# Performance work log

Measured on AMD Instinct MI355X. Metric: run time of the kernel, lower is better.

## Reference

```python
import jax, jax.numpy as jnp
from jax import lax
import numpy as np

B, S, T = 128, 256, 256
VOCAB, EMBED, ENC, DEC, DOF, LOOKBACK = 32000, 256, 256, 512, 4, 4


def setup_inputs() -> dict:
    key = jax.random.key(0)
    ks = jax.random.split(key, 20)
    w = lambda k, shape: jax.random.normal(k, shape, jnp.float32) * 0.05
    return {
        "in_seq": jax.random.randint(ks[0], (B, S), 0, VOCAB),
        "tgt_seq": jax.random.normal(ks[1], (B, T, DOF), jnp.float32),
        "lengths": jnp.full((B,), S, dtype=jnp.int32),
        "embedding": w(ks[2], (VOCAB, EMBED)),
        "enc_Wih_f": w(ks[3], (4 * ENC, EMBED)),
        "enc_Whh_f": w(ks[4], (4 * ENC, ENC)),
        "enc_b_f": w(ks[5], (4 * ENC,)),
        "enc_Wih_b": w(ks[6], (4 * ENC, EMBED)),
        "enc_Whh_b": w(ks[7], (4 * ENC, ENC)),
        "enc_b_b": w(ks[8], (4 * ENC,)),
        "dec_Wih": w(ks[9], (4 * DEC, DEC + LOOKBACK * DOF)),
        "dec_Whh": w(ks[10], (4 * DEC, DEC)),
        "dec_b": w(ks[11], (4 * DEC,)),
        "W_src": w(ks[12], (DEC, 2 * ENC)),
        "W_ctx": w(ks[13], (DEC, 2 * ENC + DEC)),
        "W_out": w(ks[14], (DOF, DEC)),
        "b_out": w(ks[15], (DOF,)),
    }


def _lstm_cell(x, h, c, Wih, Whh, b):
    # PyTorch gate order: i, f, g, o
    g = x @ Wih.T + h @ Whh.T + b
    i, f, gg, o = jnp.split(g, 4, axis=-1)
    c_new = jax.nn.sigmoid(f) * c + jax.nn.sigmoid(i) * jnp.tanh(gg)
    h_new = jax.nn.sigmoid(o) * jnp.tanh(c_new)
    return h_new, c_new


def _scan_lstm(xs, Wih, Whh, b, reverse=False):
    # xs: [T, B, E] -> hidden states [T, B, H] (aligned to original time order)
    Bsz, H = xs.shape[1], Whh.shape[1]
    h0 = jnp.zeros((Bsz, H), xs.dtype)

    def step(carry, x):
        h, c = carry
        h, c = _lstm_cell(x, h, c, Wih, Whh, b)
        return (h, c), h

    _, hs = lax.scan(step, (h0, h0), xs, reverse=reverse)
    return hs


def reference(in_seq, tgt_seq, lengths, embedding,
              enc_Wih_f, enc_Whh_f, enc_b_f,
              enc_Wih_b, enc_Whh_b, enc_b_b,
              dec_Wih, dec_Whh, dec_b,
              W_src, W_ctx, W_out, b_out):
    Bsz, Tlen = tgt_seq.shape[0], tgt_seq.shape[1]
    # ----- encoder (bi-LSTM, eval mode: dropout off, zero initial state) -----
    emb = embedding[in_seq]              # [B,S,E]
    xs = jnp.swapaxes(emb, 0, 1)         # [S,B,E]
    hf = _scan_lstm(xs, enc_Wih_f, enc_Whh_f, enc_b_f, reverse=False)
    hb = _scan_lstm(xs, enc_Wih_b, enc_Whh_b, enc_b_b, reverse=True)
    enc_out = jnp.swapaxes(jnp.concatenate([hf, hb], axis=-1), 0, 1)  # [B,S,2H]
    enc_mask = (in_seq == 0)             # [B,S]
    # precompute attention source projection once (same math as per-step)
    proj = jnp.einsum('bse,de->bsd', enc_out, W_src)  # [B,S,DEC]
    # ----- teacher-forced lookback windows of target frames -----
    pad = jnp.concatenate([jnp.zeros((Bsz, LOOKBACK, DOF), tgt_seq.dtype), tgt_seq], axis=1)
    win = jnp.stack([pad[:, k:k + Tlen] for k in range(LOOKBACK)], axis=2)  # [B,T,LB,DOF]
    win = win.reshape(Bsz, Tlen, LOOKBACK * DOF)
    win_t = jnp.swapaxes(win, 0, 1)      # [T,B,LB*DOF]
    h0 = jnp.zeros((Bsz, DEC), tgt_seq.dtype)

    def step(carry, w_t):
        h, c, feed = carry
        x = jnp.concatenate([w_t, feed], axis=-1)         # [B, LB*DOF + DEC]
        h, c = _lstm_cell(x, h, c, dec_Wih, dec_Whh, dec_b)
        scores = jnp.einsum('bd,bsd->bs', h, proj)        # Luong general score
        scores = jnp.where(enc_mask, -jnp.inf, scores)
        aw = jax.nn.softmax(scores, axis=-1)              # [B,S]
        ctx = jnp.einsum('bs,bse->be', aw, enc_out)       # [B,2H]
        feed = jnp.tanh(jnp.concatenate([h, ctx], axis=-1) @ W_ctx.T)
        out = feed @ W_out.T + b_out                      # [B,DOF]
        return (h, c, feed), (out, aw)

    _, (outs, aws) = lax.scan(step, (h0, h0, h0), win_t)
    dec_outputs = jnp.swapaxes(outs, 0, 1)   # [B,T,DOF]
    attn_weights = jnp.swapaxes(aws, 0, 1)   # [B,T,S]
    outputs = jnp.concatenate(
        [jnp.tanh(dec_outputs[..., :-1]), jax.nn.relu(dec_outputs[..., -1:])], axis=-1)
    return outputs, attn_weights
```

## Files before the change

kernel.cpp:

```cpp
#include <hip/hip_runtime.h>
#include <stdint.h>

#define B 128
#define S 256
#define T 256
#define EMBED 256
#define ENC 256
#define DEC 512
#define DOF 4

typedef __attribute__((ext_vector_type(8))) short bf16x8;
typedef __attribute__((ext_vector_type(4))) float f32x4;

static __device__ __forceinline__ float bf2f(unsigned short u){
  union{uint32_t u;float f;}c; c.u = ((uint32_t)u)<<16; return c.f;
}
static __device__ __forceinline__ unsigned short f2bf(float f){
  union{float f;uint32_t u;}c; c.f=f; uint32_t u=c.u;
  u += 0x7fffu + ((u>>16)&1u);
  return (unsigned short)(u>>16);
}
static __device__ __forceinline__ void unp2(uint32_t w, float&a, float&b){
  union{uint32_t u;float f;}c1,c2; c1.u = w<<16; c2.u = w & 0xffff0000u; a=c1.f; b=c2.f;
}
static __device__ __forceinline__ float sigm(float x){ return 1.0f/(1.0f+__expf(-x)); }

static __device__ __forceinline__ unsigned long long ldc8(const void* p){
  return __hip_atomic_load((unsigned long long*)p, __ATOMIC_RELAXED, __HIP_MEMORY_SCOPE_AGENT);
}
static __device__ __forceinline__ void stc8(void* p, unsigned long long v){
  __hip_atomic_store((unsigned long long*)p, v, __ATOMIC_RELAXED, __HIP_MEMORY_SCOPE_AGENT);
}
static __device__ __forceinline__ void stc4(void* p, unsigned v){
  __hip_atomic_store((unsigned*)p, v, __ATOMIC_RELAXED, __HIP_MEMORY_SCOPE_AGENT);
}
static __device__ __forceinline__ void stc4f(float* p, float v){
  __hip_atomic_store((unsigned*)p, __float_as_uint(v), __ATOMIC_RELAXED, __HIP_MEMORY_SCOPE_AGENT);
}
static __device__ __forceinline__ float ldc4f(const float* p){
  return __uint_as_float(__hip_atomic_load((const unsigned*)p, __ATOMIC_RELAXED, __HIP_MEMORY_SCOPE_AGENT));
}
union F16x8 { unsigned long long q[2]; bf16x8 v; unsigned short s[8]; };
union Ubf   { bf16x8 v; uint32_t u[4]; unsigned short s[8]; };
static __device__ __forceinline__ bf16x8 ldfrag_c(const unsigned short* p){
  F16x8 u; u.q[0] = ldc8(p); u.q[1] = ldc8(p + 4); return u.v;
}
static __device__ __forceinline__ unsigned long long pack4bf(float a,float b,float c,float d){
  return (unsigned long long)f2bf(a) | ((unsigned long long)f2bf(b)<<16)
       | ((unsigned long long)f2bf(c)<<32) | ((unsigned long long)f2bf(d)<<48);
}

#define CLINE 32
#define A_OFF 0
#define C_OFF 64
#define F_OFF 128
#define PAIR_OFF 192
#define ENC_OFF 320
static __device__ __forceinline__ unsigned* cl(unsigned* c, int line){ return c + (size_t)line*CLINE; }

static __device__ __forceinline__ void bar_arr(unsigned* line){
  __builtin_amdgcn_s_waitcnt(0);
  __syncthreads();
  if (threadIdx.x == 0)
    __hip_atomic_fetch_add(line, 1u, __ATOMIC_RELAXED, __HIP_MEMORY_SCOPE_AGENT);
}
static __device__ __forceinline__ void barw(unsigned* set, unsigned target, int mask){
  if (threadIdx.x < 64){
    unsigned* p = set + (size_t)(threadIdx.x & mask)*CLINE;
    while (!__all((int)(__hip_atomic_load(p, __ATOMIC_RELAXED, __HIP_MEMORY_SCOPE_AGENT) >= target)))
      __builtin_amdgcn_s_sleep(1);
  }
  __syncthreads();
  asm volatile("" ::: "memory");
}
static __device__ __forceinline__ void pair_sync(unsigned* line, unsigned target){
  __builtin_amdgcn_s_waitcnt(0);
  __syncthreads();
  if (threadIdx.x == 0){
    __hip_atomic_fetch_add(line, 1u, __ATOMIC_RELAXED, __HIP_MEMORY_SCOPE_AGENT);
    while (__hip_atomic_load(line, __ATOMIC_RELAXED, __HIP_MEMORY_SCOPE_AGENT) < target)
      __builtin_amdgcn_s_sleep(1);
  }
  __syncthreads();
  asm volatile("" ::: "memory");
}

static __device__ __forceinline__ int enc_idx(int s, int c){
  return s*256 + (((c & 24) | ((c ^ s) & 7)) << 3);
}

__global__ __launch_bounds__(256,1) void k_encoder(
  const unsigned short* __restrict__ emb,
  const unsigned short* __restrict__ WF, const unsigned short* __restrict__ WB,
  const float* __restrict__ bF, const float* __restrict__ bB,
  unsigned short* __restrict__ hEnc,
  unsigned short* __restrict__ encOut,
  unsigned* __restrict__ cntBase)
{
  __shared__ __align__(16) unsigned short Ws[16*520];
  __shared__ __align__(16) float Gs[64*17];
  __shared__ float bsh[16];
  const int bid = blockIdx.x;
  const int dir = bid >> 7;
  const int mg  = (bid >> 6) & 1;
  const int ng  = bid & 63;
  const int tid = threadIdx.x;
  const int lane = tid & 63, w = tid >> 6;
  const int l16 = lane & 15, qd = lane >> 4;
  const int m_base = mg * 64;
  unsigned* mycnt = cntBase + (size_t)dir*16*CLINE;
  unsigned* myline = cl(mycnt, bid & 15);

  const unsigned short* Wg = (dir ? WB : WF) + (size_t)ng*16*512;
  for (int i = tid; i < 16*64; i += 256){
    const int r = i >> 6, s = i & 63;
    *(uint4*)&Ws[r*520 + s*8] = *(const uint4*)&Wg[r*512 + s*8];
  }
  if (tid < 16) bsh[tid] = (dir ? bB : bF)[ng*16 + tid];
  float c[4] = {0.f,0.f,0.f,0.f};
  __syncthreads();

  for (int t = 0; t < S; ++t){
    const int tt = dir ? (S-1-t) : t;
    const unsigned short* Ae = emb + ((size_t)tt*B + m_base + w*16 + l16)*256 + qd*8;
    bf16x8 av[8];
#pragma unroll
    for (int ks = 0; ks < 8; ++ks) av[ks] = *(const bf16x8*)(Ae + ks*32);
    if (t) barw(mycnt, (unsigned)(8u*(unsigned)t), 15);
    const unsigned short* Ah = hEnc + (((size_t)dir*2 + (size_t)(t&1))*B + m_base + w*16 + l16)*256 + qd*8;
    bf16x8 hf[8];
#pragma unroll
    for (int ks = 0; ks < 8; ++ks) hf[ks] = ldfrag_c(Ah + ks*32);
    f32x4 acc = (f32x4){0.f,0.f,0.f,0.f};
#pragma unroll
    for (int ks = 0; ks < 8; ++ks){
      bf16x8 bb = *(const bf16x8*)&Ws[l16*520 + ks*32 + qd*8];
      acc = __builtin_amdgcn_mfma_f32_16x16x32_bf16(av[ks], bb, acc, 0, 0, 0);
    }
#pragma unroll
    for (int ks = 0; ks < 8; ++ks){
      bf16x8 bb = *(const bf16x8*)&Ws[l16*520 + 256 + ks*32 + qd*8];
      acc = __builtin_amdgcn_mfma_f32_16x16x32_bf16(hf[ks], bb, acc, 0, 0, 0);
    }
    __syncthreads();
#pragma unroll
    for (int r = 0; r < 4; ++r)
      Gs[(w*16 + qd*4 + r)*17 + l16] = acc[r];
    __syncthreads();
    if (tid < 64){
      const int bl = tid;
      float hv[4];
#pragma unroll
      for (int u = 0; u < 4; ++u){
        const float gi = Gs[bl*17 + u*4 + 0] + bsh[u*4 + 0];
        const float gf = Gs[bl*17 + u*4 + 1] + bsh[u*4 + 1];
        const float gg = Gs[bl*17 + u*4 + 2] + bsh[u*4 + 2];
        const float go = Gs[bl*17 + u*4 + 3] + bsh[u*4 + 3];
        const float cn = sigm(gf)*c[u] + sigm(gi)*tanhf(gg);
        c[u] = cn;
        hv[u] = sigm(go)*tanhf(cn);
      }
      const int b2 = m_base + bl;
      const unsigned long long hq = pack4bf(hv[0],hv[1],hv[2],hv[3]);
      stc8(&hEnc[(((size_t)dir*2 + (size_t)((t+1)&1))*B + b2)*256 + ng*4], hq);
      *(unsigned long long*)&encOut[((size_t)b2*S + tt)*512 + dir*256 + ng*4] = hq;
    }
    bar_arr(myline);
  }
}

__global__ __launch_bounds__(256,2) void k_proj(
  const unsigned short* __restrict__ encOut,
  const unsigned short* __restrict__ WSP,
  unsigned short* __restrict__ proj)
{
  const int nb = blockIdx.x & 7;
  const int mt = blockIdx.x >> 3;
  const int tid = threadIdx.x;
  const int lane = tid & 63, w = tid >> 6;
  const int l16 = lane & 15, qd = lane >> 4;
  const int m0 = mt*64 + w*16;
  const unsigned short* Ap = encOut + ((size_t)m0 + l16)*512 + qd*8;
  bf16x8 av[16];
#pragma unroll
  for (int ks = 0; ks < 16; ++ks) av[ks] = *(const bf16x8*)(Ap + ks*32);
  for (int nn = 0; nn < 4; ++nn){
    const int qn = nb*4 + nn;
    const unsigned short* Bq = WSP + (size_t)qn*16*512 + (size_t)lane*8;
    f32x4 acc = (f32x4){0.f,0.f,0.f,0.f};
#pragma unroll
    for (int ks = 0; ks < 16; ++ks){
      bf16x8 bb = *(const bf16x8*)(Bq + (size_t)ks*512);
      acc = __builtin_amdgcn_mfma_f32_16x16x32_bf16(av[ks], bb, acc, 0, 0, 0);
    }
    const int d = qn*16 + l16, dh = d >> 8, dl = d & 255;
#pragma unroll
    for (int r = 0; r < 4; ++r){
      const int m = m0 + qd*4 + r;
      const int bb2 = m >> 8, s = m & 255;
      proj[(((size_t)bb2*2 + dh)*256 + s)*256 + dl] = f2bf(acc[r]);
    }
  }
}

__global__ __launch_bounds__(256,1) void k_decoder(
  const unsigned short* __restrict__ win,
  const unsigned short* __restrict__ WDx,
  const float* __restrict__ bD,
  const unsigned short* __restrict__ WCx,
  const unsigned short* __restrict__ projq,
  const unsigned short* __restrict__ encOut,
  const int* __restrict__ in_seq,
  const float* __restrict__ Wout, const float* __restrict__ bout,
  unsigned short* __restrict__ hdec,
  unsigned short* __restrict__ feed,
  unsigned short* __restrict__ ctxb,
  float* __restrict__ scp,
  float* __restrict__ out_main, float* __restrict__ out_attn,
  unsigned* __restrict__ cnts)
{
  __shared__ __align__(16) unsigned short encS[65536];
  __shared__ __align__(16) float scrf[1600];
  __shared__ float bsh[16];
  const int bid = blockIdx.x;
  const int b  = bid >> 1, eh = bid & 1;
  const int mg = bid & 1, ng = (bid >> 1) & 127;
  const int tid = threadIdx.x;
  const int lane = tid & 63, w = tid >> 6;
  const int l16 = lane & 15, qd = lane >> 4;
  const int m_base = mg*64;

  if (tid < 16) bsh[tid] = bD[ng*16 + tid];
  const int mymask = (in_seq[b*S + tid] == 0);
  {
    const unsigned short* Pq = projq + (((size_t)b*2 + eh)*256)*256;
    for (int i = 0; i < 32; ++i){
      const int s = i*8 + (tid>>5), cc = tid & 31;
      const uint4 v = *(const uint4*)&Pq[(size_t)s*256 + cc*8];
      *(uint4*)&encS[enc_idx(s, cc)] = v;
    }
  }
  bf16x8 ev[32];
  {
    const int cc = lane & 31, par = lane >> 5;
    const unsigned short* Ep = encOut + ((size_t)b*S)*512 + eh*256 + cc*8;
#pragma unroll
    for (int i2 = 0; i2 < 32; ++i2)
      ev[i2] = *(const bf16x8*)(Ep + (size_t)(w*64 + i2*2 + par)*512);
  }
  float c[4] = {0.f,0.f,0.f,0.f};
  __syncthreads();

  for (int t = 0; t < T; ++t){
    const int row = m_base + w*16 + l16;
    const unsigned short* Aw = win  + ((size_t)t*B + row)*64 + qd*8;
    const unsigned short* Af = feed + (size_t)row*512 + qd*8;
    const unsigned short* Ah = hdec + ((size_t)(t&1)*B + row)*512 + qd*8;
    const unsigned short* Bp = WDx + (size_t)ng*34*512 + (size_t)lane*8;
    f32x4 acc = (f32x4){0.f,0.f,0.f,0.f};
#pragma unroll
    for (int ch = 0; ch < 2; ++ch){
      bf16x8 hv[8];
#pragma unroll
      for (int i = 0; i < 8; ++i) hv[i] = ldfrag_c(Ah + (ch*8 + i)*32);
#pragma unroll
      for (int ks = 0; ks < 8; ++ks){
        bf16x8 bb = *(const bf16x8*)(Bp + (size_t)(18 + ch*8 + ks)*512);
        acc = __builtin_amdgcn_mfma_f32_16x16x32_bf16(hv[ks], bb, acc, 0, 0, 0);
      }
    }
    bf16x8 a0 = *(const bf16x8*)(Aw);
    bf16x8 a1 = *(const bf16x8*)(Aw + 32);
    if (t){
      if (bid & 1) barw(cl(cnts, F_OFF), (unsigned)t, 63);
      else         barw(cl(cnts, F_OFF), (unsigned)t, 31);
    }
    {
      bf16x8 b0 = *(const bf16x8*)(Bp);
      bf16x8 b1 = *(const bf16x8*)(Bp + 512);
      acc = __builtin_amdgcn_mfma_f32_16x16x32_bf16(a0, b0, acc, 0, 0, 0);
      acc = __builtin_amdgcn_mfma_f32_16x16x32_bf16(a1, b1, acc, 0, 0, 0);
    }
#pragma unroll
    for (int ch = 0; ch < 2; ++ch){
      bf16x8 av[8], bv[8];
#pragma unroll
      for (int i = 0; i < 8; ++i){
        av[i] = ldfrag_c(Af + (ch*8 + i)*32);
        bv[i] = *(const bf16x8*)(Bp + (size_t)(2 + ch*8 + i)*512);
      }
#pragma unroll
      for (int ks = 0; ks < 8; ++ks)
        acc = __builtin_amdgcn_mfma_f32_16x16x32_bf16(av[ks], bv[ks], acc, 0, 0, 0);
    }
    __syncthreads();
#pragma unroll
    for (int r = 0; r < 4; ++r)
      scrf[(w*16 + qd*4 + r)*17 + l16] = acc[r];
    __syncthreads();
    if (tid < 64){
      float hv[4];
#pragma unroll
      for (int u = 0; u < 4; ++u){
        const float gi = scrf[tid*17 + u*4 + 0] + bsh[u*4 + 0];
        const float gf = scrf[tid*17 + u*4 + 1] + bsh[u*4 + 1];
        const float gg = scrf[tid*17 + u*4 + 2] + bsh[u*4 + 2];
        const float go = scrf[tid*17 + u*4 + 3] + bsh[u*4 + 3];
        const float cn = sigm(gf)*c[u] + sigm(gi)*tanhf(gg);
        c[u] = cn;
        hv[u] = sigm(go)*tanhf(cn);
      }
      stc8(&hdec[((size_t)((t+1)&1)*B + m_base + tid)*512 + ng*4],
           pack4bf(hv[0],hv[1],hv[2],hv[3]));
    }
    bar_arr(cl(cnts, A_OFF + (bid & 63)));

    if ((bid & 1) && t > 0){
      const int b2o = bid >> 1;
      const int d = tid >> 6, kk = lane;
      const unsigned short* fp = feed + (size_t)b2o*512 + kk*8;
      F16x8 u; u.q[0] = ldc8(fp); u.q[1] = ldc8(fp + 4);
      const float* wp = Wout + d*512 + kk*8;
      float p = 0.f;
#pragma unroll
      for (int j2 = 0; j2 < 8; ++j2) p += bf2f(u.s[j2]) * wp[j2];
#pragma unroll
      for (int off = 32; off > 0; off >>= 1) p += __shfl_down(p, off, 64);
      if (kk == 0){
        const float v = p + bout[d];
        out_main[((size_t)b2o*T + (t-1))*4 + d] = (d < 3) ? tanhf(v) : fmaxf(v, 0.f);
      }
    }

    barw(cl(cnts, A_OFF), (unsigned)(4u*(unsigned)(t+1)), 63);
    if (tid < 64){
      F16x8 uq; uq.q[0] = ldc8(hdec + ((size_t)((t+1)&1)*B + b)*512 + eh*256 + tid*4);
      scrf[tid*4+0] = bf2f(uq.s[0]); scrf[tid*4+1] = bf2f(uq.s[1]);
      scrf[tid*4+2] = bf2f(uq.s[2]); scrf[tid*4+3] = bf2f(uq.s[3]);
    }
    __syncthreads();
    float sc = 0.f;
#pragma unroll 8
    for (int cix = 0; cix < 32; ++cix){
      Ubf u8; u8.v = *(const bf16x8*)&encS[enc_idx(tid, cix)];
      float f0,f1,f2,f3,f4,f5,f6,f7;
      unp2(u8.u[0],f0,f1); unp2(u8.u[1],f2,f3); unp2(u8.u[2],f4,f5); unp2(u8.u[3],f6,f7);
      const float* qp = &scrf[cix*8];
      sc += f0*qp[0] + f1*qp[1] + f2*qp[2] + f3*qp[3]
          + f4*qp[4] + f5*qp[5] + f6*qp[6] + f7*qp[7];
    }
    stc4f(&scp[((size_t)b*2 + eh)*256 + tid], sc);
    pair_sync(cl(cnts, PAIR_OFF + b), (unsigned)(2u*(unsigned)(t+1)));
    float tot = sc + ldc4f(&scp[((size_t)b*2 + (1-eh))*256 + tid]);
    if (mymask) tot = -1e30f;
    float mx = tot;
#pragma unroll
    for (int off = 32; off > 0; off >>= 1) mx = fmaxf(mx, __shfl_xor(mx, off, 64));
    if (lane == 0) scrf[512 + w] = mx;
    __syncthreads();
    mx = fmaxf(fmaxf(scrf[512], scrf[513]), fmaxf(scrf[514], scrf[515]));
    const float e = __expf(tot - mx);
    float l = e;
#pragma unroll
    for (int off = 32; off > 0; off >>= 1) l += __shfl_xor(l, off, 64);
    if (lane == 0) scrf[516 + w] = l;
    __syncthreads();
    l = scrf[516] + scrf[517] + scrf[518] + scrf[519];
    const float aw = e / l;
    scrf[256 + tid] = aw;
    if (eh == 0) __builtin_nontemporal_store(aw, &out_attn[((size_t)b*T + t)*S + tid]);
    __syncthreads();
    {
      float a[8] = {0,0,0,0,0,0,0,0};
      const int cc = lane & 31, par = lane >> 5;
#pragma unroll
      for (int i2 = 0; i2 < 32; ++i2){
        const int srow = w*64 + i2*2 + par;
        const float wgt = scrf[256 + srow];
        Ubf u8; u8.v = ev[i2];
        float f0,f1,f2,f3,f4,f5,f6,f7;
        unp2(u8.u[0],f0,f1); unp2(u8.u[1],f2,f3); unp2(u8.u[2],f4,f5); unp2(u8.u[3],f6,f7);
        a[0]+=wgt*f0; a[1]+=wgt*f1; a[2]+=wgt*f2; a[3]+=wgt*f3;
        a[4]+=wgt*f4; a[5]+=wgt*f5; a[6]+=wgt*f6; a[7]+=wgt*f7;
      }
#pragma unroll
      for (int j2 = 0; j2 < 8; ++j2) a[j2] += __shfl_xor(a[j2], 32, 64);
      if (par == 0){
#pragma unroll
        for (int j2 = 0; j2 < 8; ++j2) scrf[528 + w*256 + cc*8 + j2] = a[j2];
      }
    }
    __syncthreads();
    if (tid < 128){
      const int e2 = tid*2;
      const float s0 = scrf[528+e2]     + scrf[528+256+e2]     + scrf[528+512+e2]     + scrf[528+768+e2];
      const float s1 = scrf[528+e2+1]   + scrf[528+256+e2+1]   + scrf[528+512+e2+1]   + scrf[528+768+e2+1];
      stc4(&ctxb[(size_t)b*512 + eh*256 + e2],
           (unsigned)f2bf(s0) | ((unsigned)f2bf(s1) << 16));
    }
    bar_arr(cl(cnts, C_OFF + (bid & 63)));

    if ((bid & 3) == 3){
      const int fblk = bid >> 2, fm = fblk >> 5, fn = fblk & 31;
      const int frow = fm*64 + w*16 + l16;
      const unsigned short* Fh = hdec + ((size_t)((t+1)&1)*B + frow)*512 + qd*8;
      const unsigned short* Fc = ctxb + (size_t)frow*512 + qd*8;
      const unsigned short* Bf = WCx + (size_t)fn*32*512 + (size_t)lane*8;
      f32x4 fa = (f32x4){0.f,0.f,0.f,0.f};
#pragma unroll
      for (int ch = 0; ch < 2; ++ch){
        bf16x8 av[8], bv[8];
#pragma unroll
        for (int i = 0; i < 8; ++i){
          av[i] = ldfrag_c(Fh + (ch*8 + i)*32);
          bv[i] = *(const bf16x8*)(Bf + (size_t)(ch*8 + i)*512);
        }
#pragma unroll
        for (int ks = 0; ks < 8; ++ks)
          fa = __builtin_amdgcn_mfma_f32_16x16x32_bf16(av[ks], bv[ks], fa, 0, 0, 0);
      }
      barw(cl(cnts, C_OFF), (unsigned)(4u*(unsigned)(t+1)), 63);
#pragma unroll
      for (int ch = 0; ch < 2; ++ch){
        bf16x8 av[8], bv[8];
#pragma unroll
        for (int i = 0; i < 8; ++i){
          av[i] = ldfrag_c(Fc + (ch*8 + i)*32);
          bv[i] = *(const bf16x8*)(Bf + (size_t)(16 + ch*8 + i)*512);
        }
#pragma unroll
        for (int ks = 0; ks < 8; ++ks)
          fa = __builtin_amdgcn_mfma_f32_16x16x32_bf16(av[ks], bv[ks], fa, 0, 0, 0);
      }
      __syncthreads();
#pragma unroll
      for (int r = 0; r < 4; ++r)
        scrf[(w*16 + qd*4 + r)*17 + l16] = tanhf(fa[r]);
      __syncthreads();
      if (tid < 64){
        const int fb = fm*64 + tid;
#pragma unroll
        for (int u = 0; u < 4; ++u)
          stc8(&feed[(size_t)fb*512 + fn*16 + u*4],
               pack4bf(scrf[tid*17+u*4+0], scrf[tid*17+u*4+1],
                       scrf[tid*17+u*4+2], scrf[tid*17+u*4+3]));
      }
      bar_arr(cl(cnts, F_OFF + (bid >> 2)));
    }
  }
  if (bid & 1){
    barw(cl(cnts, F_OFF), 256u, 63);
    const int b2o = bid >> 1;
    const int d = tid >> 6, kk = lane;
    const unsigned short* fp = feed + (size_t)b2o*512 + kk*8;
    F16x8 u; u.q[0] = ldc8(fp); u.q[1] = ldc8(fp + 4);
    const float* wp = Wout + d*512 + kk*8;
    float p = 0.f;
#pragma unroll
    for (int j2 = 0; j2 < 8; ++j2) p += bf2f(u.s[j2]) * wp[j2];
#pragma unroll
    for (int off = 32; off > 0; off >>= 1) p += __shfl_down(p, off, 64);
    if (kk == 0){
      const float v = p + bout[d];
      out_main[((size_t)b2o*T + 255)*4 + d] = (d < 3) ? tanhf(v) : fmaxf(v, 0.f);
    }
  }
}

__global__ __launch_bounds__(256) void k_build_encw(
  const float* __restrict__ WihF, const float* __restrict__ WhhF,
  const float* __restrict__ WihB, const float* __restrict__ WhhB,
  unsigned short* WF, unsigned short* WB)
{
  const int idx = blockIdx.x*256 + threadIdx.x;
  const int dir = idx >> 19;
  const int i2 = idx & 524287;
  const int row = i2 >> 9, col = i2 & 511;
  const int j = row >> 2, g = row & 3;
  const int orig = g*256 + j;
  const float* Wih = dir ? WihB : WihF;
  const float* Whh = dir ? WhhB : WhhF;
  const float v = (col < 256) ? Wih[orig*256 + col] : Whh[orig*256 + (col-256)];
  (dir ? WB : WF)[i2] = f2bf(v);
}

__global__ __launch_bounds__(256) void k_build_decw(
  const float* __restrict__ Wih, const float* __restrict__ Whh, unsigned short* WDx)
{
  const int idx = blockIdx.x*256 + threadIdx.x;
  if (idx >= 2048*1088) return;
  const int row = idx / 1088, col = idx - row*1088;
  const int j = row >> 2, g = row & 3;
  const int orig = g*512 + j;
  float v;
  if (col < 16)        v = Wih[orig*528 + col];
  else if (col < 64)   v = 0.f;
  else if (col < 576)  v = Wih[orig*528 + (col - 48)];
  else                 v = Whh[orig*512 + (col - 576)];
  const int ng = row >> 4, l16 = row & 15;
  const int ks = col >> 5, qdd = (col >> 3) & 3, jj = col & 7;
  WDx[(((size_t)ng*34 + ks)*64 + qdd*16 + l16)*8 + jj] = f2bf(v);
}

__global__ __launch_bounds__(256) void k_build_wcx(
  const float* __restrict__ Wctx, unsigned short* WCx)
{
  const int idx = blockIdx.x*256 + threadIdx.x;
  const int n = idx >> 10, k = idx & 1023;
  const int fn = n >> 4, l16 = n & 15;
  const int ks = k >> 5, qdd = (k >> 3) & 3, jj = k & 7;
  WCx[(((size_t)fn*32 + ks)*64 + qdd*16 + l16)*8 + jj] = f2bf(Wctx[(size_t)n*1024 + k]);
}

__global__ __launch_bounds__(256) void k_build_wsp(
  const float* __restrict__ Wsrc, unsigned short* WSP)
{
  const int idx = blockIdx.x*256 + threadIdx.x;
  const int d = idx >> 9, e = idx & 511;
  const int qn = d >> 4, l16 = d & 15;
  const int ks = e >> 5, qdd = (e >> 3) & 3, jj = e & 7;
  WSP[(((size_t)qn*16 + ks)*64 + qdd*16 + l16)*8 + jj] = f2bf(Wsrc[(size_t)d*512 + e]);
}

__global__ __launch_bounds__(256) void k_build_bias(
  const float* __restrict__ ebF, const float* __restrict__ ebB,
  const float* __restrict__ dB, float* bF, float* bB, float* bD)
{
  const int idx = blockIdx.x*256 + threadIdx.x;
  if (idx < 1024) bF[idx] = ebF[(idx&3)*256 + (idx>>2)];
  else if (idx < 2048){ const int i = idx-1024; bB[i] = ebB[(i&3)*256 + (i>>2)]; }
  else { const int i = idx-2048; bD[i] = dB[(i&3)*512 + (i>>2)]; }
}

__global__ __launch_bounds__(256) void k_embed(
  const int* __restrict__ in_seq, const float* __restrict__ table, unsigned short* emb)
{
  const int idx = blockIdx.x*256 + threadIdx.x;
  const int e = idx & 255, b = (idx >> 8) & 127, s = idx >> 15;
  const int tok = in_seq[b*S + s];
  emb[idx] = f2bf(table[(size_t)tok*256 + e]);
}

__global__ __launch_bounds__(256) void k_win(
  const float* __restrict__ tgt, unsigned short* win)
{
  const int idx = blockIdx.x*256 + threadIdx.x;
  const int c = idx & 63, b = (idx >> 6) & 127, t = idx >> 13;
  float v = 0.f;
  if (c < 16){
    const int k = c >> 2, jj = c & 3;
    const int ts = t + k - 4;
    if (ts >= 0) v = tgt[((size_t)b*T + ts)*4 + jj];
  }
  win[idx] = f2bf(v);
}

extern "C" void kernel_launch(void* const* d_in, const int* in_sizes, int n_in,
                              void* d_out, int out_size, void* d_ws, size_t ws_size,
                              hipStream_t stream)
{
  const int*   in_seq    = (const int*)d_in[0];
  const float* tgt       = (const float*)d_in[1];
  const float* embedding = (const float*)d_in[3];
  const float* eWihF = (const float*)d_in[4];
  const float* eWhhF = (const float*)d_in[5];
  const float* ebF   = (const float*)d_in[6];
  const float* eWihB = (const float*)d_in[7];
  const float* eWhhB = (const float*)d_in[8];
  const float* ebB   = (const float*)d_in[9];
  const float* dWih  = (const float*)d_in[10];
  const float* dWhh  = (const float*)d_in[11];
  const float* dB    = (const float*)d_in[12];
  const float* Wsrc  = (const float*)d_in[13];
  const float* Wctx  = (const float*)d_in[14];
  const float* Wout  = (const float*)d_in[15];
  const float* bout  = (const float*)d_in[16];

  char* ws = (char*)d_ws;
  size_t off = 0;
  auto al = [&](size_t bytes)->char*{
    char* p = ws + off; off += (bytes + 255) & ~(size_t)255; return p; };

  char* stateBase = ws;
  unsigned short* hEnc = (unsigned short*)al(262144);
  unsigned short* hdec = (unsigned short*)al(262144);
  unsigned short* feed = (unsigned short*)al(131072);
  unsigned short* ctxb = (unsigned short*)al(131072);
  unsigned*       cnts = (unsigned*)al(45056);
  const size_t stateBytes = off;

  unsigned short* emb    = (unsigned short*)al(16777216);
  unsigned short* win    = (unsigned short*)al(4194304);
  unsigned short* encOut = (unsigned short*)al(33554432);
  unsigned short* proj   = (unsigned short*)al(33554432);
  unsigned short* WF     = (unsigned short*)al(1048576);
  unsigned short* WB     = (unsigned short*)al(1048576);
  unsigned short* WDx    = (unsigned short*)al(4456448);
  unsigned short* WCx    = (unsigned short*)al(1048576);
  unsigned short* WSP    = (unsigned short*)al(524288);
  float*          scp    = (float*)al(262144);
  float* bFr = (float*)al(4096);
  float* bBr = (float*)al(4096);
  float* bDr = (float*)al(8192);
  (void)ws_size; (void)in_sizes; (void)n_in; (void)out_size;

  float* out_main = (float*)d_out;
  float* out_attn = out_main + (size_t)B*T*DOF;

  const dim3 blk(256);
  k_build_encw <<<4096,  blk, 0, stream>>>(eWihF, eWhhF, eWihB, eWhhB, WF, WB);
  k_build_decw <<<8704,  blk, 0, stream>>>(dWih, dWhh, WDx);
  k_build_wcx  <<<2048,  blk, 0, stream>>>(Wctx, WCx);
  k_build_wsp  <<<1024,  blk, 0, stream>>>(Wsrc, WSP);
  k_build_bias <<<16,    blk, 0, stream>>>(ebF, ebB, dB, bFr, bBr, bDr);
  k_embed      <<<32768, blk, 0, stream>>>(in_seq, embedding, emb);
  k_win        <<<8192,  blk, 0, stream>>>(tgt, win);
  hipMemsetAsync(stateBase, 0, stateBytes, stream);

  k_encoder<<<256, blk, 0, stream>>>(emb, WF, WB, bFr, bBr, hEnc, encOut,
                                     cnts + (size_t)ENC_OFF*CLINE);

  k_proj<<<4096, blk, 0, stream>>>(encOut, WSP, proj);

  k_decoder<<<256, blk, 0, stream>>>(win, WDx, bDr, WCx, proj, encOut, in_seq,
                                     Wout, bout, hdec, feed, ctxb, scp,
                                     out_main, out_attn, cnts);
}
```

Before: 8.888 ms.

## Fold context projection into encoder outputs and compute feed per batch row

The ctx half of W_ctx is now pre-multiplied into the encoder outputs (encW = enc_out·W_ctx_ctxᵀ) in the projection kernel, so the attention-weighted sum yields the ctx contribution to feed directly. The h half is computed per block with a scalar dot over the full decoder hidden state, overlapped with the pair-sync wait. This removes the separate ctx buffer, one grid-wide barrier and the MFMA feed GEMM each timestep, at the cost of a second 32MB precomputed tensor and more per-block scalar work. The feed barrier target changes to count four arrivals per step.

```diff
diff --git a/kernel.cpp b/kernel.cpp
--- a/kernel.cpp
+++ b/kernel.cpp
@@ -52,7 +52,6 @@
 
 #define CLINE 32
 #define A_OFF 0
-#define C_OFF 64
 #define F_OFF 128
 #define PAIR_OFF 192
 #define ENC_OFF 320
@@ -68,17 +67,6 @@
   if (threadIdx.x < 64){
     unsigned* p = set + (size_t)(threadIdx.x & mask)*CLINE;
     while (!__all((int)(__hip_atomic_load(p, __ATOMIC_RELAXED, __HIP_MEMORY_SCOPE_AGENT) >= target)))
-      __builtin_amdgcn_s_sleep(1);
-  }
-  __syncthreads();
-  asm volatile("" ::: "memory");
-}
-static __device__ __forceinline__ void pair_sync(unsigned* line, unsigned target){
-  __builtin_amdgcn_s_waitcnt(0);
-  __syncthreads();
-  if (threadIdx.x == 0){
-    __hip_atomic_fetch_add(line, 1u, __ATOMIC_RELAXED, __HIP_MEMORY_SCOPE_AGENT);
-    while (__hip_atomic_load(line, __ATOMIC_RELAXED, __HIP_MEMORY_SCOPE_AGENT) < target)
       __builtin_amdgcn_s_sleep(1);
   }
   __syncthreads();
@@ -172,7 +160,9 @@
 __global__ __launch_bounds__(256,2) void k_proj(
   const unsigned short* __restrict__ encOut,
   const unsigned short* __restrict__ WSP,
-  unsigned short* __restrict__ proj)
+  const unsigned short* __restrict__ WCP,
+  unsigned short* __restrict__ proj,
+  unsigned short* __restrict__ encW)
 {
   const int nb = blockIdx.x & 7;
   const int mt = blockIdx.x >> 3;
@@ -184,21 +174,25 @@
   bf16x8 av[16];
 #pragma unroll
   for (int ks = 0; ks < 16; ++ks) av[ks] = *(const bf16x8*)(Ap + ks*32);
-  for (int nn = 0; nn < 4; ++nn){
-    const int qn = nb*4 + nn;
-    const unsigned short* Bq = WSP + (size_t)qn*16*512 + (size_t)lane*8;
-    f32x4 acc = (f32x4){0.f,0.f,0.f,0.f};
-#pragma unroll
-    for (int ks = 0; ks < 16; ++ks){
-      bf16x8 bb = *(const bf16x8*)(Bq + (size_t)ks*512);
-      acc = __builtin_amdgcn_mfma_f32_16x16x32_bf16(av[ks], bb, acc, 0, 0, 0);
-    }
-    const int d = qn*16 + l16, dh = d >> 8, dl = d & 255;
-#pragma unroll
-    for (int r = 0; r < 4; ++r){
-      const int m = m0 + qd*4 + r;
-      const int bb2 = m >> 8, s = m & 255;
-      proj[(((size_t)bb2*2 + dh)*256 + s)*256 + dl] = f2bf(acc[r]);
+  for (int which = 0; which < 2; ++which){
+    const unsigned short* Wb = which ? WCP : WSP;
+    unsigned short* outp = which ? encW : proj;
+    for (int nn = 0; nn < 4; ++nn){
+      const int qn = nb*4 + nn;
+      const unsigned short* Bq = Wb + (size_t)qn*16*512 + (size_t)lane*8;
+      f32x4 acc = (f32x4){0.f,0.f,0.f,0.f};
+#pragma unroll
+      for (int ks = 0; ks < 16; ++ks){
+        bf16x8 bb = *(const bf16x8*)(Bq + (size_t)ks*512);
+        acc = __builtin_amdgcn_mfma_f32_16x16x32_bf16(av[ks], bb, acc, 0, 0, 0);
+      }
+      const int d = qn*16 + l16, dh = d >> 8, dl = d & 255;
+#pragma unroll
+      for (int r = 0; r < 4; ++r){
+        const int m = m0 + qd*4 + r;
+        const int bb2 = m >> 8, s = m & 255;
+        outp[(((size_t)bb2*2 + dh)*256 + s)*256 + dl] = f2bf(acc[r]);
+      }
     }
   }
 }
@@ -207,20 +201,19 @@
   const unsigned short* __restrict__ win,
   const unsigned short* __restrict__ WDx,
   const float* __restrict__ bD,
-  const unsigned short* __restrict__ WCx,
+  const unsigned short* __restrict__ WhP,
   const unsigned short* __restrict__ projq,
-  const unsigned short* __restrict__ encOut,
+  const unsigned short* __restrict__ encWq,
   const int* __restrict__ in_seq,
   const float* __restrict__ Wout, const float* __restrict__ bout,
   unsigned short* __restrict__ hdec,
   unsigned short* __restrict__ feed,
-  unsigned short* __restrict__ ctxb,
   float* __restrict__ scp,
   float* __restrict__ out_main, float* __restrict__ out_attn,
   unsigned* __restrict__ cnts)
 {
   __shared__ __align__(16) unsigned short encS[65536];
-  __shared__ __align__(16) float scrf[1600];
+  __shared__ __align__(16) float scrf[2080];
   __shared__ float bsh[16];
   const int bid = blockIdx.x;
   const int b  = bid >> 1, eh = bid & 1;
@@ -243,10 +236,10 @@
   bf16x8 ev[32];
   {
     const int cc = lane & 31, par = lane >> 5;
-    const unsigned short* Ep = encOut + ((size_t)b*S)*512 + eh*256 + cc*8;
+    const unsigned short* Ep = encWq + (((size_t)b*2 + eh)*256)*256 + cc*8;
 #pragma unroll
     for (int i2 = 0; i2 < 32; ++i2)
-      ev[i2] = *(const bf16x8*)(Ep + (size_t)(w*64 + i2*2 + par)*512);
+      ev[i2] = *(const bf16x8*)(Ep + (size_t)(w*64 + i2*2 + par)*256);
   }
   float c[4] = {0.f,0.f,0.f,0.f};
   __syncthreads();
@@ -272,8 +265,8 @@
     bf16x8 a0 = *(const bf16x8*)(Aw);
     bf16x8 a1 = *(const bf16x8*)(Aw + 32);
     if (t){
-      if (bid & 1) barw(cl(cnts, F_OFF), (unsigned)t, 63);
-      else         barw(cl(cnts, F_OFF), (unsigned)t, 31);
+      if (bid & 1) barw(cl(cnts, F_OFF), (unsigned)(4u*(unsigned)t), 63);
+      else         barw(cl(cnts, F_OFF), (unsigned)(4u*(unsigned)t), 31);
     }
     {
       bf16x8 b0 = *(const bf16x8*)(Bp);
@@ -334,9 +327,10 @@
 
     barw(cl(cnts, A_OFF), (unsigned)(4u*(unsigned)(t+1)), 63);
     if (tid < 64){
-      F16x8 uq; uq.q[0] = ldc8(hdec + ((size_t)((t+1)&1)*B + b)*512 + eh*256 + tid*4);
-      scrf[tid*4+0] = bf2f(uq.s[0]); scrf[tid*4+1] = bf2f(uq.s[1]);
-      scrf[tid*4+2] = bf2f(uq.s[2]); scrf[tid*4+3] = bf2f(uq.s[3]);
+      const unsigned short* hp = hdec + ((size_t)((t+1)&1)*B + b)*512 + tid*8;
+      F16x8 uh; uh.q[0] = ldc8(hp); uh.q[1] = ldc8(hp + 4);
+#pragma unroll
+      for (int j = 0; j < 8; ++j) scrf[tid*8 + j] = bf2f(uh.s[j]);
     }
     __syncthreads();
     float sc = 0.f;
@@ -345,29 +339,56 @@
       Ubf u8; u8.v = *(const bf16x8*)&encS[enc_idx(tid, cix)];
       float f0,f1,f2,f3,f4,f5,f6,f7;
       unp2(u8.u[0],f0,f1); unp2(u8.u[1],f2,f3); unp2(u8.u[2],f4,f5); unp2(u8.u[3],f6,f7);
-      const float* qp = &scrf[cix*8];
+      const float* qp = &scrf[eh*256 + cix*8];
       sc += f0*qp[0] + f1*qp[1] + f2*qp[2] + f3*qp[3]
           + f4*qp[4] + f5*qp[5] + f6*qp[6] + f7*qp[7];
     }
     stc4f(&scp[((size_t)b*2 + eh)*256 + tid], sc);
-    pair_sync(cl(cnts, PAIR_OFF + b), (unsigned)(2u*(unsigned)(t+1)));
+    __builtin_amdgcn_s_waitcnt(0);
+    __syncthreads();
+    if (tid == 0)
+      __hip_atomic_fetch_add(cl(cnts, PAIR_OFF + b), 1u, __ATOMIC_RELAXED, __HIP_MEMORY_SCOPE_AGENT);
+    float hw0 = 0.f, hw1 = 0.f, hw2 = 0.f, hw3 = 0.f;
+    {
+      const unsigned short* Wp = WhP + (size_t)(eh*256 + tid)*8;
+#pragma unroll 8
+      for (int kc = 0; kc < 64; ++kc){
+        Ubf u8; u8.v = *(const bf16x8*)(Wp + (size_t)kc*4096);
+        const float4 h0 = *(const float4*)&scrf[kc*8];
+        const float4 h1 = *(const float4*)&scrf[kc*8 + 4];
+        float f0,f1,f2,f3,f4,f5,f6,f7;
+        unp2(u8.u[0],f0,f1); unp2(u8.u[1],f2,f3); unp2(u8.u[2],f4,f5); unp2(u8.u[3],f6,f7);
+        hw0 += h0.x*f0 + h1.x*f4;
+        hw1 += h0.y*f1 + h1.y*f5;
+        hw2 += h0.z*f2 + h1.z*f6;
+        hw3 += h0.w*f3 + h1.w*f7;
+      }
+    }
+    const float hw = (hw0 + hw1) + (hw2 + hw3);
+    if (tid == 0){
+      unsigned* pp = cl(cnts, PAIR_OFF + b);
+      while (__hip_atomic_load(pp, __ATOMIC_RELAXED, __HIP_MEMORY_SCOPE_AGENT) < 2u*(unsigned)(t+1))
+        __builtin_amdgcn_s_sleep(1);
+    }
+    __syncthreads();
+    asm volatile("" ::: "memory");
     float tot = sc + ldc4f(&scp[((size_t)b*2 + (1-eh))*256 + tid]);
     if (mymask) tot = -1e30f;
     float mx = tot;
 #pragma unroll
     for (int off = 32; off > 0; off >>= 1) mx = fmaxf(mx, __shfl_xor(mx, off, 64));
-    if (lane == 0) scrf[512 + w] = mx;
-    __syncthreads();
-    mx = fmaxf(fmaxf(scrf[512], scrf[513]), fmaxf(scrf[514], scrf[515]));
+    if (lane == 0) scrf[768 + w] = mx;
+    __syncthreads();
+    mx = fmaxf(fmaxf(scrf[768], scrf[769]), fmaxf(scrf[770], scrf[771]));
     const float e = __expf(tot - mx);
     float l = e;
 #pragma unroll
     for (int off = 32; off > 0; off >>= 1) l += __shfl_xor(l, off, 64);
-    if (lane == 0) scrf[516 + w] = l;
-    __syncthreads();
-    l = scrf[516] + scrf[517] + scrf[518] + scrf[519];
+    if (lane == 0) scrf[772 + w] = l;
+    __syncthreads();
+    l = scrf[772] + scrf[773] + scrf[774] + scrf[775];
     const float aw = e / l;
-    scrf[256 + tid] = aw;
+    scrf[512 + tid] = aw;
     if (eh == 0) __builtin_nontemporal_store(aw, &out_attn[((size_t)b*T + t)*S + tid]);
     __syncthreads();
     {
@@ -376,7 +397,7 @@
 #pragma unroll
       for (int i2 = 0; i2 < 32; ++i2){
         const int srow = w*64 + i2*2 + par;
-        const float wgt = scrf[256 + srow];
+        const float wgt = scrf[512 + srow];
         Ubf u8; u8.v = ev[i2];
         float f0,f1,f2,f3,f4,f5,f6,f7;
         unp2(u8.u[0],f0,f1); unp2(u8.u[1],f2,f3); unp2(u8.u[2],f4,f5); unp2(u8.u[3],f6,f7);
@@ -387,69 +408,25 @@
       for (int j2 = 0; j2 < 8; ++j2) a[j2] += __shfl_xor(a[j2], 32, 64);
       if (par == 0){
 #pragma unroll
-        for (int j2 = 0; j2 < 8; ++j2) scrf[528 + w*256 + cc*8 + j2] = a[j2];
-      }
+        for (int j2 = 0; j2 < 8; ++j2) scrf[784 + w*256 + cc*8 + j2] = a[j2];
+      }
+    }
+    __syncthreads();
+    {
+      const float v = scrf[784 + tid] + scrf[784 + 256 + tid]
+                    + scrf[784 + 512 + tid] + scrf[784 + 768 + tid];
+      scrf[1808 + tid] = tanhf(hw + v);
     }
     __syncthreads();
     if (tid < 128){
-      const int e2 = tid*2;
-      const float s0 = scrf[528+e2]     + scrf[528+256+e2]     + scrf[528+512+e2]     + scrf[528+768+e2];
-      const float s1 = scrf[528+e2+1]   + scrf[528+256+e2+1]   + scrf[528+512+e2+1]   + scrf[528+768+e2+1];
-      stc4(&ctxb[(size_t)b*512 + eh*256 + e2],
-           (unsigned)f2bf(s0) | ((unsigned)f2bf(s1) << 16));
-    }
-    bar_arr(cl(cnts, C_OFF + (bid & 63)));
-
-    if ((bid & 3) == 3){
-      const int fblk = bid >> 2, fm = fblk >> 5, fn = fblk & 31;
-      const int frow = fm*64 + w*16 + l16;
-      const unsigned short* Fh = hdec + ((size_t)((t+1)&1)*B + frow)*512 + qd*8;
-      const unsigned short* Fc = ctxb + (size_t)frow*512 + qd*8;
-      const unsigned short* Bf = WCx + (size_t)fn*32*512 + (size_t)lane*8;
-      f32x4 fa = (f32x4){0.f,0.f,0.f,0.f};
-#pragma unroll
-      for (int ch = 0; ch < 2; ++ch){
-        bf16x8 av[8], bv[8];
-#pragma unroll
-        for (int i = 0; i < 8; ++i){
-          av[i] = ldfrag_c(Fh + (ch*8 + i)*32);
-          bv[i] = *(const bf16x8*)(Bf + (size_t)(ch*8 + i)*512);
-        }
-#pragma unroll
-        for (int ks = 0; ks < 8; ++ks)
-          fa = __builtin_amdgcn_mfma_f32_16x16x32_bf16(av[ks], bv[ks], fa, 0, 0, 0);
-      }
-      barw(cl(cnts, C_OFF), (unsigned)(4u*(unsigned)(t+1)), 63);
-#pragma unroll
-      for (int ch = 0; ch < 2; ++ch){
-        bf16x8 av[8], bv[8];
-#pragma unroll
-        for (int i = 0; i < 8; ++i){
-          av[i] = ldfrag_c(Fc + (ch*8 + i)*32);
-          bv[i] = *(const bf16x8*)(Bf + (size_t)(16 + ch*8 + i)*512);
-        }
-#pragma unroll
-        for (int ks = 0; ks < 8; ++ks)
-          fa = __builtin_amdgcn_mfma_f32_16x16x32_bf16(av[ks], bv[ks], fa, 0, 0, 0);
-      }
-      __syncthreads();
-#pragma unroll
-      for (int r = 0; r < 4; ++r)
-        scrf[(w*16 + qd*4 + r)*17 + l16] = tanhf(fa[r]);
-      __syncthreads();
-      if (tid < 64){
-        const int fb = fm*64 + tid;
-#pragma unroll
-        for (int u = 0; u < 4; ++u)
-          stc8(&feed[(size_t)fb*512 + fn*16 + u*4],
-               pack4bf(scrf[tid*17+u*4+0], scrf[tid*17+u*4+1],
-                       scrf[tid*17+u*4+2], scrf[tid*17+u*4+3]));
-      }
-      bar_arr(cl(cnts, F_OFF + (bid >> 2)));
-    }
+      const int n2 = tid*2;
+      stc4(&feed[(size_t)b*512 + eh*256 + n2],
+           (unsigned)f2bf(scrf[1808 + n2]) | ((unsigned)f2bf(scrf[1808 + n2 + 1]) << 16));
+    }
+    bar_arr(cl(cnts, F_OFF + (bid >> 2)));
   }
   if (bid & 1){
-    barw(cl(cnts, F_OFF), 256u, 63);
+    barw(cl(cnts, F_OFF), (unsigned)(4u*256u), 63);
     const int b2o = bid >> 1;
     const int d = tid >> 6, kk = lane;
     const unsigned short* fp = feed + (size_t)b2o*512 + kk*8;
@@ -502,14 +479,22 @@
   WDx[(((size_t)ng*34 + ks)*64 + qdd*16 + l16)*8 + jj] = f2bf(v);
 }
 
-__global__ __launch_bounds__(256) void k_build_wcx(
-  const float* __restrict__ Wctx, unsigned short* WCx)
-{
-  const int idx = blockIdx.x*256 + threadIdx.x;
-  const int n = idx >> 10, k = idx & 1023;
-  const int fn = n >> 4, l16 = n & 15;
-  const int ks = k >> 5, qdd = (k >> 3) & 3, jj = k & 7;
-  WCx[(((size_t)fn*32 + ks)*64 + qdd*16 + l16)*8 + jj] = f2bf(Wctx[(size_t)n*1024 + k]);
+__global__ __launch_bounds__(256) void k_build_whp(
+  const float* __restrict__ Wctx, unsigned short* WhP)
+{
+  const int idx = blockIdx.x*256 + threadIdx.x;
+  const int k = idx >> 9, n = idx & 511;
+  WhP[(((size_t)(k >> 3)*512 + n) << 3) + (k & 7)] = f2bf(Wctx[(size_t)n*1024 + k]);
+}
+
+__global__ __launch_bounds__(256) void k_build_wcp(
+  const float* __restrict__ Wctx, unsigned short* WCP)
+{
+  const int idx = blockIdx.x*256 + threadIdx.x;
+  const int n = idx >> 9, e = idx & 511;
+  const int qn = n >> 4, l16 = n & 15;
+  const int ks = e >> 5, qdd = (e >> 3) & 3, jj = e & 7;
+  WCP[(((size_t)qn*16 + ks)*64 + qdd*16 + l16)*8 + jj] = f2bf(Wctx[(size_t)n*1024 + 512 + e]);
 }
 
 __global__ __launch_bounds__(256) void k_build_wsp(
@@ -585,7 +570,6 @@
   unsigned short* hEnc = (unsigned short*)al(262144);
   unsigned short* hdec = (unsigned short*)al(262144);
   unsigned short* feed = (unsigned short*)al(131072);
-  unsigned short* ctxb = (unsigned short*)al(131072);
   unsigned*       cnts = (unsigned*)al(45056);
   const size_t stateBytes = off;
 
@@ -593,10 +577,12 @@
   unsigned short* win    = (unsigned short*)al(4194304);
   unsigned short* encOut = (unsigned short*)al(33554432);
   unsigned short* proj   = (unsigned short*)al(33554432);
+  unsigned short* encWq  = (unsigned short*)al(33554432);
   unsigned short* WF     = (unsigned short*)al(1048576);
   unsigned short* WB     = (unsigned short*)al(1048576);
   unsigned short* WDx    = (unsigned short*)al(4456448);
-  unsigned short* WCx    = (unsigned short*)al(1048576);
+  unsigned short* WhP    = (unsigned short*)al(524288);
+  unsigned short* WCP    = (unsigned short*)al(524288);
   unsigned short* WSP    = (unsigned short*)al(524288);
   float*          scp    = (float*)al(262144);
   float* bFr = (float*)al(4096);
@@ -610,7 +596,8 @@
   const dim3 blk(256);
   k_build_encw <<<4096,  blk, 0, stream>>>(eWihF, eWhhF, eWihB, eWhhB, WF, WB);
   k_build_decw <<<8704,  blk, 0, stream>>>(dWih, dWhh, WDx);
-  k_build_wcx  <<<2048,  blk, 0, stream>>>(Wctx, WCx);
+  k_build_whp  <<<1024,  blk, 0, stream>>>(Wctx, WhP);
+  k_build_wcp  <<<1024,  blk, 0, stream>>>(Wctx, WCP);
   k_build_wsp  <<<1024,  blk, 0, stream>>>(Wsrc, WSP);
   k_build_bias <<<16,    blk, 0, stream>>>(ebF, ebB, dB, bFr, bBr, bDr);
   k_embed      <<<32768, blk, 0, stream>>>(in_seq, embedding, emb);
@@ -620,9 +607,9 @@
   k_encoder<<<256, blk, 0, stream>>>(emb, WF, WB, bFr, bBr, hEnc, encOut,
                                      cnts + (size_t)ENC_OFF*CLINE);
 
-  k_proj<<<4096, blk, 0, stream>>>(encOut, WSP, proj);
-
-  k_decoder<<<256, blk, 0, stream>>>(win, WDx, bDr, WCx, proj, encOut, in_seq,
-                                     Wout, bout, hdec, feed, ctxb, scp,
+  k_proj<<<4096, blk, 0, stream>>>(encOut, WSP, WCP, proj, encWq);
+
+  k_decoder<<<256, blk, 0, stream>>>(win, WDx, bDr, WhP, proj, encWq, in_seq,
+                                     Wout, bout, hdec, feed, scp,
                                      out_main, out_attn, cnts);
 }
```

Measured after the change: 8.830 ms. No clear change (-0.7%).
